# Performance work log

Hardware: AMD Instinct MI355X
Metric: run time of the kernel (lower is better)

Reference implementation:

```python
import jax, jax.numpy as jnp
import numpy as np
from jax import lax

SEQ, BATCH, IN_W = 2048, 64, 256
STREAM_W = 1024
OUT_W = 64


def _range(num, lo, hi):
    return np.arange(num, dtype=np.float64) / float(num - 1) * (hi - lo) + lo


def _sin_buffers(width):
    # Faithful to ResSin: tau = 2*pi, w_min = -2*tau, w_max = 2*tau
    tau = 2.0 * np.pi
    w_max = 2.0 * tau
    l_num = width // 2
    r_num = width - l_num
    inner = np.concatenate([
        _range(l_num, -w_max, -1.0 / l_num),
        _range(r_num, 1.0 / r_num, w_max),
    ])
    outer = np.concatenate([
        _range(l_num, -1.0, -w_max),
        _range(r_num, w_max, 1.0),
    ]) / inner
    return inner.astype(np.float32), outer.astype(np.float32)


def setup_inputs() -> dict:
    key = jax.random.key(0)
    ks = jax.random.split(key, 7)
    W = STREAM_W
    inner, outer = _sin_buffers(W)
    scale = 1.0 / np.sqrt(W)
    return {
        "input": jax.random.normal(ks[0], (SEQ, BATCH, IN_W), dtype=jnp.float32),
        "initial_stream": jax.random.normal(ks[1], (W,), dtype=jnp.float32) * 0.02,
        "w1": jax.random.normal(ks[2], (W, W), dtype=jnp.float32) * scale,
        "b1": jax.random.normal(ks[3], (W,), dtype=jnp.float32) * 0.01,
        "w2": jax.random.normal(ks[4], (W, W), dtype=jnp.float32) * scale,
        "b2": jax.random.normal(ks[5], (W,), dtype=jnp.float32) * 0.01,
        "bendiness": jax.random.normal(ks[6], (W,), dtype=jnp.float32) * 0.1,
        "inner_weight": jnp.asarray(inner),
        "outer_weight": jnp.asarray(outer),
    }


def reference(input, initial_stream, w1, b1, w2, b2, bendiness, inner_weight, outer_weight):
    S, B, I = input.shape
    W = initial_stream.shape[0]
    pad = W - I
    stream0 = jnp.broadcast_to(initial_stream, (B, W))

    def step(stream, elem):
        # Add: pad input element up to stream width and add residually
        s = stream + jnp.pad(elem, ((0, 0), (0, pad)))
        # ResLinear fc1: addmm(bias, x, weight.T)
        h = s @ w1.T + b1
        # ResSin: x + bendiness * outer * sin(x * inner)
        h = h + bendiness * outer_weight * jnp.sin(h * inner_weight)
        # ResLinear fc2
        s = h @ w2.T + b2
        return s, None

    final, _ = lax.scan(step, stream0, input)
    # seq_indices = -1 (default): every batch element takes the last stream
    outputs = final[:, :OUT_W]
    return outputs, final
```

## Files before the change

### kernel.cpp

```cpp
#include <hip/hip_runtime.h>
#include <math.h>


#define WDIM 1024
#define SEQ_N 2048
#define NB 256
#define LDS_BYTES 163840

__device__ __forceinline__ double gload(const double* p) {
  unsigned long long v = __hip_atomic_load((const unsigned long long*)p,
                                           __ATOMIC_RELAXED, __HIP_MEMORY_SCOPE_AGENT);
  return __builtin_bit_cast(double, v);
}
__device__ __forceinline__ void gstore(double* p, double d) {
  __hip_atomic_store((unsigned long long*)p, __builtin_bit_cast(unsigned long long, d),
                     __ATOMIC_RELAXED, __HIP_MEMORY_SCOPE_AGENT);
}

__device__ __forceinline__ void gbar(unsigned* bar, unsigned target, int leaf) {
  __syncthreads();
  if (threadIdx.x == 0) {
    __builtin_amdgcn_fence(__ATOMIC_RELEASE, "agent");
    unsigned old = __hip_atomic_fetch_add(&bar[32 + leaf * 16], 1u, __ATOMIC_RELAXED,
                                          __HIP_MEMORY_SCOPE_AGENT);
    if (old + 1u == target * 16u) {
      unsigned r = __hip_atomic_fetch_add(&bar[16], 1u, __ATOMIC_RELAXED,
                                          __HIP_MEMORY_SCOPE_AGENT);
      if (r + 1u == target * 16u)
        __hip_atomic_store(&bar[0], target, __ATOMIC_RELAXED, __HIP_MEMORY_SCOPE_AGENT);
    }
    while (__hip_atomic_load(&bar[0], __ATOMIC_RELAXED, __HIP_MEMORY_SCOPE_AGENT) < target)
      __builtin_amdgcn_s_sleep(2);
  }
  __syncthreads();
}

__global__ __launch_bounds__(256) void k_gemm_wt(const float* __restrict__ A,
                                                 const float* __restrict__ B,
                                                 double* __restrict__ Wcd) {
  __shared__ float As[32][68];
  __shared__ float Bs[32][68];
  const int tid = threadIdx.x;
  const int tx = tid & 15, ty = tid >> 4;
  const int bx = blockIdx.x, by = blockIdx.y;
  double acc[4][4] = {};
  for (int j0 = 0; j0 < WDIM; j0 += 32) {
    for (int l = tid; l < 64 * 32; l += 256) {
      int r = l >> 5, c = l & 31;
      As[c][r] = A[(by * 64 + r) * WDIM + j0 + c];
    }
    for (int l = tid; l < 32 * 64; l += 256) {
      int r = l >> 6, c = l & 63;
      Bs[r][c] = B[(j0 + r) * WDIM + bx * 64 + c];
    }
    __syncthreads();
#pragma unroll 8
    for (int kk = 0; kk < 32; ++kk) {
      float a[4], bb[4];
      *(float4*)a  = *(const float4*)&As[kk][ty * 4];
      *(float4*)bb = *(const float4*)&Bs[kk][tx * 4];
#pragma unroll
      for (int i = 0; i < 4; ++i)
#pragma unroll
        for (int j = 0; j < 4; ++j) acc[i][j] += (double)a[i] * (double)bb[j];
    }
    __syncthreads();
  }
#pragma unroll
  for (int i = 0; i < 4; ++i)
#pragma unroll
    for (int j = 0; j < 4; ++j)
      Wcd[(size_t)(by * 64 + ty * 4 + i) * WDIM + bx * 64 + tx * 4 + j] = acc[i][j];
}

__global__ __launch_bounds__(256) void k_bias(const float* __restrict__ W1,
                                              const float* __restrict__ b1,
                                              const float* __restrict__ b2,
                                              const float* __restrict__ s0,
                                              double* __restrict__ b1c,
                                              double* __restrict__ c0, unsigned* bar) {
  if (blockIdx.x < 2) {
    int i = blockIdx.x * 256 + threadIdx.x;
    if (i < 288) bar[i] = 0u;
  }
  int wave = threadIdx.x >> 6;
  int lane = threadIdx.x & 63;
  int n = blockIdx.x * 4 + wave;
  const float* row = W1 + (size_t)n * WDIM;
  double a1 = 0.0, a2 = 0.0;
  for (int k = lane; k < WDIM; k += 64) {
    double w = (double)row[k];
    a1 += (double)b2[k] * w;
    a2 += (double)s0[k] * w;
  }
#pragma unroll
  for (int off = 32; off; off >>= 1) {
    a1 += __shfl_down(a1, off, 64);
    a2 += __shfl_down(a2, off, 64);
  }
  if (lane == 0) { b1c[n] = (double)b1[n] + a1; c0[n] = (double)b1[n] + a2; }
}

__global__ __launch_bounds__(512, 2) void k_main(
    const float* __restrict__ x, const double* __restrict__ Wcd,
    const float* __restrict__ W1, const double* __restrict__ b1c,
    const double* __restrict__ c0, const float* __restrict__ W2,
    const float* __restrict__ b2, const float* __restrict__ bend,
    const float* __restrict__ inner, const float* __restrict__ outer,
    double* vA, double* vB, float* __restrict__ out, unsigned* bar) {
  extern __shared__ double2 tile[];
  double* red = (double*)(tile + 8192);
  const int tid = threadIdx.x;
  const int ks = tid & 31;
  const int bg = (tid >> 5) & 3;
  const int ng = (tid >> 7) & 3;
  const int nt = blockIdx.x & 63, g = blockIdx.x >> 6;
  const int leaf = blockIdx.x >> 4;

  if (tid < 256) vA[blockIdx.x * 256 + tid] = 0.0;

  const double* wrow[4];
  const float* w1row[4];
  const float* w2row[4];
#pragma unroll
  for (int jn = 0; jn < 4; ++jn) {
    int n = nt * 16 + ng * 4 + jn;
    wrow[jn]  = Wcd + (size_t)n * WDIM;
    w1row[jn] = W1 + (size_t)n * WDIM;
    w2row[jn] = W2 + (size_t)n * WDIM;
  }

  const int n_red = nt * 16 + (tid & 15);
  const int b_red = g * 16 + ((tid >> 4) & 15);
  const double bo   = (double)bend[n_red] * (double)outer[n_red];
  const double inw  = (double)inner[n_red];
  const double b1cr = b1c[n_red];
  const double c0r  = c0[n_red];
  const int oswz = (ng * 4) & 15;

  unsigned gent = 0;
  double* vin = vA;
  double* vout = vB;
  gbar(bar, ++gent, leaf);

  for (int t = 0; t < SEQ_N; ++t) {
    float2 xv[4][4], wv[4][4];
#pragma unroll
    for (int i = 0; i < 4; ++i) {
      int c2 = i * 32 + ks;
#pragma unroll
      for (int r = 0; r < 4; ++r)
        xv[r][i] = ((const float2*)(x + ((size_t)t * 64 + g * 16 + bg * 4 + r) * 256))[c2];
#pragma unroll
      for (int jn = 0; jn < 4; ++jn)
        wv[jn][i] = ((const float2*)w1row[jn])[c2];
    }
    double va[16], vb[16];
    {
      const double* srcb = vin + (size_t)(g * 16) * WDIM + tid * 2;
#pragma unroll
      for (int j = 0; j < 16; ++j) {
        va[j] = gload(srcb + (size_t)j * WDIM);
        vb[j] = gload(srcb + (size_t)j * WDIM + 1);
      }
    }

    double accx[4][4], accy[4][4];
#pragma unroll
    for (int ib = 0; ib < 4; ++ib)
#pragma unroll
      for (int jn = 0; jn < 4; ++jn) { accx[ib][jn] = 0.0; accy[ib][jn] = 0.0; }
#pragma unroll
    for (int i = 0; i < 4; ++i)
#pragma unroll
      for (int jn = 0; jn < 4; ++jn) {
        double wx = (double)wv[jn][i].x, wy = (double)wv[jn][i].y;
        accx[0][jn] += (double)xv[0][i].x * wx; accy[0][jn] += (double)xv[0][i].y * wy;
        accx[1][jn] += (double)xv[1][i].x * wx; accy[1][jn] += (double)xv[1][i].y * wy;
        accx[2][jn] += (double)xv[2][i].x * wx; accy[2][jn] += (double)xv[2][i].y * wy;
        accx[3][jn] += (double)xv[3][i].x * wx; accy[3][jn] += (double)xv[3][i].y * wy;
      }

#pragma unroll
    for (int j = 0; j < 16; ++j)
      tile[j * 512 + tid] = make_double2(va[j], vb[j]);
    __syncthreads();

#pragma unroll 4
    for (int i = 0; i < 16; ++i) {
      int c2 = i * 32 + ks;
      double2 v0 = tile[(bg * 4 + 0) * 512 + c2];
      double2 v1 = tile[(bg * 4 + 1) * 512 + c2];
      double2 v2 = tile[(bg * 4 + 2) * 512 + c2];
      double2 v3 = tile[(bg * 4 + 3) * 512 + c2];
#pragma unroll
      for (int jn = 0; jn < 4; ++jn) {
        double2 w = ((const double2*)wrow[jn])[c2];
        accx[0][jn] += v0.x * w.x; accy[0][jn] += v0.y * w.y;
        accx[1][jn] += v1.x * w.x; accy[1][jn] += v1.y * w.y;
        accx[2][jn] += v2.x * w.x; accy[2][jn] += v2.y * w.y;
        accx[3][jn] += v3.x * w.x; accy[3][jn] += v3.y * w.y;
      }
    }

#pragma unroll
    for (int ib = 0; ib < 4; ++ib)
#pragma unroll
      for (int jn = 0; jn < 4; ++jn) {
        double p = accx[ib][jn] + accy[ib][jn];
        p += __shfl_xor(p, 16, 64);
        if (ks < 16) {
          int o = (bg * 4 + ib) * 16 + ng * 4 + jn;
          red[o * 16 + (ks ^ ((oswz + jn) & 15))] = p;
        }
      }
    __syncthreads();

    if (tid < 256) {
      double s = 0.0;
      const int oc = tid & 15;
#pragma unroll
      for (int slc = 0; slc < 16; ++slc)
        s += red[tid * 16 + (slc ^ oc)];
      double u = s + (t == 0 ? c0r : b1cr);
      double gv = u + bo * sin(u * inw);
      gstore(&vout[(size_t)b_red * WDIM + n_red], gv);
    }

    gbar(bar, ++gent, leaf);
    double* tmp = vin; vin = vout; vout = tmp;
  }

  {
    double va[16], vb[16];
    {
      const double* srcb = vin + (size_t)(g * 16) * WDIM + tid * 2;
#pragma unroll
      for (int j = 0; j < 16; ++j) {
        va[j] = gload(srcb + (size_t)j * WDIM);
        vb[j] = gload(srcb + (size_t)j * WDIM + 1);
      }
    }
#pragma unroll
    for (int j = 0; j < 16; ++j)
      tile[j * 512 + tid] = make_double2(va[j], vb[j]);
    __syncthreads();

    double accx[4][4], accy[4][4];
#pragma unroll
    for (int ib = 0; ib < 4; ++ib)
#pragma unroll
      for (int jn = 0; jn < 4; ++jn) { accx[ib][jn] = 0.0; accy[ib][jn] = 0.0; }

#pragma unroll 4
    for (int i = 0; i < 16; ++i) {
      int c2 = i * 32 + ks;
      double2 v0 = tile[(bg * 4 + 0) * 512 + c2];
      double2 v1 = tile[(bg * 4 + 1) * 512 + c2];
      double2 v2 = tile[(bg * 4 + 2) * 512 + c2];
      double2 v3 = tile[(bg * 4 + 3) * 512 + c2];
#pragma unroll
      for (int jn = 0; jn < 4; ++jn) {
        float2 wf = ((const float2*)w2row[jn])[c2];
        double wx = (double)wf.x, wy = (double)wf.y;
        accx[0][jn] += v0.x * wx; accy[0][jn] += v0.y * wy;
        accx[1][jn] += v1.x * wx; accy[1][jn] += v1.y * wy;
        accx[2][jn] += v2.x * wx; accy[2][jn] += v2.y * wy;
        accx[3][jn] += v3.x * wx; accy[3][jn] += v3.y * wy;
      }
    }
#pragma unroll
    for (int ib = 0; ib < 4; ++ib)
#pragma unroll
      for (int jn = 0; jn < 4; ++jn) {
        double p = accx[ib][jn] + accy[ib][jn];
        p += __shfl_xor(p, 16, 64);
        if (ks < 16) {
          int o = (bg * 4 + ib) * 16 + ng * 4 + jn;
          red[o * 16 + (ks ^ ((oswz + jn) & 15))] = p;
        }
      }
    __syncthreads();
    if (tid < 256) {
      double s = 0.0;
      const int oc = tid & 15;
#pragma unroll
      for (int slc = 0; slc < 16; ++slc)
        s += red[tid * 16 + (slc ^ oc)];
      double sv = s + (double)b2[n_red];
      out[4096 + (size_t)b_red * WDIM + n_red] = (float)sv;
      if (n_red < 64) out[(size_t)b_red * 64 + n_red] = (float)sv;
    }
  }
}

extern "C" void kernel_launch(void* const* d_in, const int* in_sizes, int n_in,
                              void* d_out, int out_size, void* d_ws, size_t ws_size,
                              hipStream_t stream) {
  const float* x    = (const float*)d_in[0];
  const float* s0   = (const float*)d_in[1];
  const float* W1   = (const float*)d_in[2];
  const float* b1   = (const float*)d_in[3];
  const float* W2   = (const float*)d_in[4];
  const float* b2   = (const float*)d_in[5];
  const float* bend = (const float*)d_in[6];
  const float* inner= (const float*)d_in[7];
  const float* outer= (const float*)d_in[8];
  double* ws = (double*)d_ws;

  double* Wcd = ws;
  double* b1c = ws + 1048576;
  double* c0  = ws + 1049600;
  double* vA  = ws + 1050624;
  double* vB  = ws + 1116160;
  unsigned* bar = (unsigned*)(ws + 1181696);
  float* out = (float*)d_out;

  k_gemm_wt<<<dim3(16, 16), 256, 0, stream>>>(W1, W2, Wcd);
  k_bias<<<256, 256, 0, stream>>>(W1, b1, b2, s0, b1c, c0, bar);

  static bool attr_done = false;
  if (!attr_done) {
    hipFuncSetAttribute((const void*)k_main,
                        hipFuncAttributeMaxDynamicSharedMemorySize, LDS_BYTES);
    attr_done = true;
  }

  void* args[] = { (void*)&x, (void*)&Wcd, (void*)&W1, (void*)&b1c, (void*)&c0,
                   (void*)&W2, (void*)&b2, (void*)&bend, (void*)&inner, (void*)&outer,
                   (void*)&vA, (void*)&vB, (void*)&out, (void*)&bar };
  hipError_t le = hipLaunchCooperativeKernel((void*)k_main, dim3(NB), dim3(512),
                                             args, LDS_BYTES, stream);
  if (le != hipSuccess) {
    k_main<<<dim3(NB), dim3(512), LDS_BYTES, stream>>>(
        x, Wcd, W1, b1c, c0, W2, b2, bend, inner, outer, vA, vB, out, bar);
  }
}
```

Baseline: 36.74 ms.

## Split cooperative kernel into per-batch-group barriers with smaller 256-thread blocks

```diff
diff --git a/kernel.cpp b/kernel.cpp
--- a/kernel.cpp
+++ b/kernel.cpp
@@ -4,8 +4,8 @@
 
 #define WDIM 1024
 #define SEQ_N 2048
-#define NB 256
-#define LDS_BYTES 163840
+#define LDS8 81920
+#define LDSL 163840
 
 __device__ __forceinline__ double gload(const double* p) {
   unsigned long long v = __hip_atomic_load((const unsigned long long*)p,
@@ -17,19 +17,20 @@
                      __ATOMIC_RELAXED, __HIP_MEMORY_SCOPE_AGENT);
 }
 
-__device__ __forceinline__ void gbar(unsigned* bar, unsigned target, int leaf) {
+__device__ __forceinline__ void gbar(unsigned* barR, unsigned target, int leaf,
+                                     unsigned perleaf, unsigned leaves) {
   __syncthreads();
   if (threadIdx.x == 0) {
     __builtin_amdgcn_fence(__ATOMIC_RELEASE, "agent");
-    unsigned old = __hip_atomic_fetch_add(&bar[32 + leaf * 16], 1u, __ATOMIC_RELAXED,
+    unsigned old = __hip_atomic_fetch_add(&barR[32 + leaf * 16], 1u, __ATOMIC_RELAXED,
                                           __HIP_MEMORY_SCOPE_AGENT);
-    if (old + 1u == target * 16u) {
-      unsigned r = __hip_atomic_fetch_add(&bar[16], 1u, __ATOMIC_RELAXED,
+    if (old + 1u == target * perleaf) {
+      unsigned r = __hip_atomic_fetch_add(&barR[16], 1u, __ATOMIC_RELAXED,
                                           __HIP_MEMORY_SCOPE_AGENT);
-      if (r + 1u == target * 16u)
-        __hip_atomic_store(&bar[0], target, __ATOMIC_RELAXED, __HIP_MEMORY_SCOPE_AGENT);
-    }
-    while (__hip_atomic_load(&bar[0], __ATOMIC_RELAXED, __HIP_MEMORY_SCOPE_AGENT) < target)
+      if (r + 1u == target * leaves)
+        __hip_atomic_store(&barR[0], target, __ATOMIC_RELAXED, __HIP_MEMORY_SCOPE_AGENT);
+    }
+    while (__hip_atomic_load(&barR[0], __ATOMIC_RELAXED, __HIP_MEMORY_SCOPE_AGENT) < target)
       __builtin_amdgcn_s_sleep(2);
   }
   __syncthreads();
@@ -79,10 +80,7 @@
                                               const float* __restrict__ s0,
                                               double* __restrict__ b1c,
                                               double* __restrict__ c0, unsigned* bar) {
-  if (blockIdx.x < 2) {
-    int i = blockIdx.x * 256 + threadIdx.x;
-    if (i < 288) bar[i] = 0u;
-  }
+  if (blockIdx.x < 16) bar[blockIdx.x * 256 + threadIdx.x] = 0u;
   int wave = threadIdx.x >> 6;
   int lane = threadIdx.x & 63;
   int n = blockIdx.x * 4 + wave;
@@ -99,6 +97,194 @@
     a2 += __shfl_down(a2, off, 64);
   }
   if (lane == 0) { b1c[n] = (double)b1[n] + a1; c0[n] = (double)b1[n] + a2; }
+}
+
+__global__ __launch_bounds__(256, 2) void k_main8(
+    const float* __restrict__ x, const double* __restrict__ Wcd,
+    const float* __restrict__ W1, const double* __restrict__ b1c,
+    const double* __restrict__ c0, const float* __restrict__ W2,
+    const float* __restrict__ b2, const float* __restrict__ bend,
+    const float* __restrict__ inner, const float* __restrict__ outer,
+    double* vA, double* vB, float* __restrict__ out, unsigned* bar) {
+  extern __shared__ double2 tile[];
+  double* red = (double*)(tile + 4096);
+  const int tid = threadIdx.x;
+  const int ks = tid & 31;
+  const int bg = (tid >> 5) & 1;
+  const int ng = tid >> 6;
+  const int nt = blockIdx.x & 63, g = blockIdx.x >> 6;
+  const int leaf = nt >> 3;
+  unsigned* barG = bar + g * 512;
+
+  if (tid < 128) vA[blockIdx.x * 128 + tid] = 0.0;
+
+  const double* wrow[4];
+  const float* w1row[4];
+  const float* w2row[4];
+#pragma unroll
+  for (int jn = 0; jn < 4; ++jn) {
+    int n = nt * 16 + ng * 4 + jn;
+    wrow[jn]  = Wcd + (size_t)n * WDIM;
+    w1row[jn] = W1 + (size_t)n * WDIM;
+    w2row[jn] = W2 + (size_t)n * WDIM;
+  }
+
+  const int n_red = nt * 16 + (tid & 15);
+  const int b_red = g * 8 + ((tid >> 4) & 7);
+  const double bo   = (double)bend[n_red] * (double)outer[n_red];
+  const double inw  = (double)inner[n_red];
+  const double b1cr = b1c[n_red];
+  const double c0r  = c0[n_red];
+  const int oswz = (ng * 4) & 15;
+
+  unsigned gent = 0;
+  double* vin = vA;
+  double* vout = vB;
+  gbar(barG, ++gent, leaf, 8u, 8u);
+
+  for (int t = 0; t < SEQ_N; ++t) {
+    float2 xv[4][4], wv[4][4];
+#pragma unroll
+    for (int i = 0; i < 4; ++i) {
+      int c2 = i * 32 + ks;
+#pragma unroll
+      for (int r = 0; r < 4; ++r)
+        xv[r][i] = ((const float2*)(x + ((size_t)t * 64 + g * 8 + bg * 4 + r) * 256))[c2];
+#pragma unroll
+      for (int jn = 0; jn < 4; ++jn)
+        wv[jn][i] = ((const float2*)w1row[jn])[c2];
+    }
+    double va[16], vb[16];
+    {
+#pragma unroll
+      for (int j = 0; j < 16; ++j) {
+        int idx = j * 256 + tid;
+        int r = idx >> 9, c2 = idx & 511;
+        const double* s = vin + (size_t)(g * 8 + r) * WDIM + c2 * 2;
+        va[j] = gload(s); vb[j] = gload(s + 1);
+      }
+    }
+    double accx[4][4], accy[4][4];
+#pragma unroll
+    for (int ib = 0; ib < 4; ++ib)
+#pragma unroll
+      for (int jn = 0; jn < 4; ++jn) { accx[ib][jn] = 0.0; accy[ib][jn] = 0.0; }
+#pragma unroll
+    for (int i = 0; i < 4; ++i)
+#pragma unroll
+      for (int jn = 0; jn < 4; ++jn) {
+        double wx = (double)wv[jn][i].x, wy = (double)wv[jn][i].y;
+        accx[0][jn] += (double)xv[0][i].x * wx; accy[0][jn] += (double)xv[0][i].y * wy;
+        accx[1][jn] += (double)xv[1][i].x * wx; accy[1][jn] += (double)xv[1][i].y * wy;
+        accx[2][jn] += (double)xv[2][i].x * wx; accy[2][jn] += (double)xv[2][i].y * wy;
+        accx[3][jn] += (double)xv[3][i].x * wx; accy[3][jn] += (double)xv[3][i].y * wy;
+      }
+#pragma unroll
+    for (int j = 0; j < 16; ++j) {
+      int idx = j * 256 + tid;
+      tile[idx] = make_double2(va[j], vb[j]);
+    }
+    __syncthreads();
+#pragma unroll 4
+    for (int i = 0; i < 16; ++i) {
+      int c2 = i * 32 + ks;
+      double2 v0 = tile[(bg * 4 + 0) * 512 + c2];
+      double2 v1 = tile[(bg * 4 + 1) * 512 + c2];
+      double2 v2 = tile[(bg * 4 + 2) * 512 + c2];
+      double2 v3 = tile[(bg * 4 + 3) * 512 + c2];
+#pragma unroll
+      for (int jn = 0; jn < 4; ++jn) {
+        double2 w = ((const double2*)wrow[jn])[c2];
+        accx[0][jn] += v0.x * w.x; accy[0][jn] += v0.y * w.y;
+        accx[1][jn] += v1.x * w.x; accy[1][jn] += v1.y * w.y;
+        accx[2][jn] += v2.x * w.x; accy[2][jn] += v2.y * w.y;
+        accx[3][jn] += v3.x * w.x; accy[3][jn] += v3.y * w.y;
+      }
+    }
+#pragma unroll
+    for (int ib = 0; ib < 4; ++ib)
+#pragma unroll
+      for (int jn = 0; jn < 4; ++jn) {
+        double p = accx[ib][jn] + accy[ib][jn];
+        p += __shfl_xor(p, 16, 64);
+        if (ks < 16) {
+          int o = (bg * 4 + ib) * 16 + ng * 4 + jn;
+          red[o * 16 + (ks ^ ((oswz + jn) & 15))] = p;
+        }
+      }
+    __syncthreads();
+    if (tid < 128) {
+      double s = 0.0;
+      const int oc = tid & 15;
+#pragma unroll
+      for (int slc = 0; slc < 16; ++slc)
+        s += red[tid * 16 + (slc ^ oc)];
+      double u = s + (t == 0 ? c0r : b1cr);
+      double gv = u + bo * sin(u * inw);
+      gstore(&vout[(size_t)b_red * WDIM + n_red], gv);
+    }
+    gbar(barG, ++gent, leaf, 8u, 8u);
+    double* tmp = vin; vin = vout; vout = tmp;
+  }
+
+  {
+    double va[16], vb[16];
+#pragma unroll
+    for (int j = 0; j < 16; ++j) {
+      int idx = j * 256 + tid;
+      int r = idx >> 9, c2 = idx & 511;
+      const double* s = vin + (size_t)(g * 8 + r) * WDIM + c2 * 2;
+      va[j] = gload(s); vb[j] = gload(s + 1);
+    }
+#pragma unroll
+    for (int j = 0; j < 16; ++j)
+      tile[j * 256 + tid] = make_double2(va[j], vb[j]);
+    __syncthreads();
+    double accx[4][4], accy[4][4];
+#pragma unroll
+    for (int ib = 0; ib < 4; ++ib)
+#pragma unroll
+      for (int jn = 0; jn < 4; ++jn) { accx[ib][jn] = 0.0; accy[ib][jn] = 0.0; }
+#pragma unroll 4
+    for (int i = 0; i < 16; ++i) {
+      int c2 = i * 32 + ks;
+      double2 v0 = tile[(bg * 4 + 0) * 512 + c2];
+      double2 v1 = tile[(bg * 4 + 1) * 512 + c2];
+      double2 v2 = tile[(bg * 4 + 2) * 512 + c2];
+      double2 v3 = tile[(bg * 4 + 3) * 512 + c2];
+#pragma unroll
+      for (int jn = 0; jn < 4; ++jn) {
+        float2 wf = ((const float2*)w2row[jn])[c2];
+        double wx = (double)wf.x, wy = (double)wf.y;
+        accx[0][jn] += v0.x * wx; accy[0][jn] += v0.y * wy;
+        accx[1][jn] += v1.x * wx; accy[1][jn] += v1.y * wy;
+        accx[2][jn] += v2.x * wx; accy[2][jn] += v2.y * wy;
+        accx[3][jn] += v3.x * wx; accy[3][jn] += v3.y * wy;
+      }
+    }
+#pragma unroll
+    for (int ib = 0; ib < 4; ++ib)
+#pragma unroll
+      for (int jn = 0; jn < 4; ++jn) {
+        double p = accx[ib][jn] + accy[ib][jn];
+        p += __shfl_xor(p, 16, 64);
+        if (ks < 16) {
+          int o = (bg * 4 + ib) * 16 + ng * 4 + jn;
+          red[o * 16 + (ks ^ ((oswz + jn) & 15))] = p;
+        }
+      }
+    __syncthreads();
+    if (tid < 128) {
+      double s = 0.0;
+      const int oc = tid & 15;
+#pragma unroll
+      for (int slc = 0; slc < 16; ++slc)
+        s += red[tid * 16 + (slc ^ oc)];
+      double sv = s + (double)b2[n_red];
+      out[4096 + (size_t)b_red * WDIM + n_red] = (float)sv;
+      if (n_red < 64) out[(size_t)b_red * 64 + n_red] = (float)sv;
+    }
+  }
 }
 
 __global__ __launch_bounds__(512, 2) void k_main(
@@ -129,7 +315,6 @@
     w1row[jn] = W1 + (size_t)n * WDIM;
     w2row[jn] = W2 + (size_t)n * WDIM;
   }
-
   const int n_red = nt * 16 + (tid & 15);
   const int b_red = g * 16 + ((tid >> 4) & 15);
   const double bo   = (double)bend[n_red] * (double)outer[n_red];
@@ -141,7 +326,7 @@
   unsigned gent = 0;
   double* vin = vA;
   double* vout = vB;
-  gbar(bar, ++gent, leaf);
+  gbar(bar, ++gent, leaf, 16u, 16u);
 
   for (int t = 0; t < SEQ_N; ++t) {
     float2 xv[4][4], wv[4][4];
@@ -164,7 +349,6 @@
         vb[j] = gload(srcb + (size_t)j * WDIM + 1);
       }
     }
-
     double accx[4][4], accy[4][4];
 #pragma unroll
     for (int ib = 0; ib < 4; ++ib)
@@ -180,12 +364,10 @@
         accx[2][jn] += (double)xv[2][i].x * wx; accy[2][jn] += (double)xv[2][i].y * wy;
         accx[3][jn] += (double)xv[3][i].x * wx; accy[3][jn] += (double)xv[3][i].y * wy;
       }
-
 #pragma unroll
     for (int j = 0; j < 16; ++j)
       tile[j * 512 + tid] = make_double2(va[j], vb[j]);
     __syncthreads();
-
 #pragma unroll 4
     for (int i = 0; i < 16; ++i) {
       int c2 = i * 32 + ks;
@@ -202,7 +384,6 @@
         accx[3][jn] += v3.x * w.x; accy[3][jn] += v3.y * w.y;
       }
     }
-
 #pragma unroll
     for (int ib = 0; ib < 4; ++ib)
 #pragma unroll
@@ -215,7 +396,6 @@
         }
       }
     __syncthreads();
-
     if (tid < 256) {
       double s = 0.0;
       const int oc = tid & 15;
@@ -226,11 +406,9 @@
       double gv = u + bo * sin(u * inw);
       gstore(&vout[(size_t)b_red * WDIM + n_red], gv);
     }
-
-    gbar(bar, ++gent, leaf);
+    gbar(bar, ++gent, leaf, 16u, 16u);
     double* tmp = vin; vin = vout; vout = tmp;
   }
-
   {
     double va[16], vb[16];
     {
@@ -245,13 +423,11 @@
     for (int j = 0; j < 16; ++j)
       tile[j * 512 + tid] = make_double2(va[j], vb[j]);
     __syncthreads();
-
     double accx[4][4], accy[4][4];
 #pragma unroll
     for (int ib = 0; ib < 4; ++ib)
 #pragma unroll
       for (int jn = 0; jn < 4; ++jn) { accx[ib][jn] = 0.0; accy[ib][jn] = 0.0; }
-
 #pragma unroll 4
     for (int i = 0; i < 16; ++i) {
       int c2 = i * 32 + ks;
@@ -321,18 +497,26 @@
 
   static bool attr_done = false;
   if (!attr_done) {
-    hipFuncSetAttribute((const void*)k_main,
-                        hipFuncAttributeMaxDynamicSharedMemorySize, LDS_BYTES);
+    hipFuncSetAttribute((const void*)k_main8, hipFuncAttributeMaxDynamicSharedMemorySize, LDS8);
+    hipFuncSetAttribute((const void*)k_main,  hipFuncAttributeMaxDynamicSharedMemorySize, LDSL);
     attr_done = true;
   }
 
   void* args[] = { (void*)&x, (void*)&Wcd, (void*)&W1, (void*)&b1c, (void*)&c0,
                    (void*)&W2, (void*)&b2, (void*)&bend, (void*)&inner, (void*)&outer,
                    (void*)&vA, (void*)&vB, (void*)&out, (void*)&bar };
-  hipError_t le = hipLaunchCooperativeKernel((void*)k_main, dim3(NB), dim3(512),
-                                             args, LDS_BYTES, stream);
-  if (le != hipSuccess) {
-    k_main<<<dim3(NB), dim3(512), LDS_BYTES, stream>>>(
-        x, Wcd, W1, b1c, c0, W2, b2, bend, inner, outer, vA, vB, out, bar);
-  }
-}
+
+  int maxB8 = 0;
+  hipError_t q8 = hipOccupancyMaxActiveBlocksPerMultiprocessor(&maxB8, k_main8, 256, LDS8);
+  if (q8 == hipSuccess && maxB8 >= 2) {
+    if (hipLaunchCooperativeKernel((void*)k_main8, dim3(512), dim3(256), args,
+                                   LDS8, stream) != hipSuccess)
+      k_main8<<<dim3(512), dim3(256), LDS8, stream>>>(
+          x, Wcd, W1, b1c, c0, W2, b2, bend, inner, outer, vA, vB, out, bar);
+  } else {
+    if (hipLaunchCooperativeKernel((void*)k_main, dim3(256), dim3(512), args,
+                                   LDSL, stream) != hipSuccess)
+      k_main<<<dim3(256), dim3(512), LDSL, stream>>>(
+          x, Wcd, W1, b1c, c0, W2, b2, bend, inner, outer, vA, vB, out, bar);
+  }
+}
```

After: 36.60 ms, median of 2. Within noise of the previous version (-0.4%).

## Replace tree grid barrier with split arrive/wait counter and overlap next-step input GEMV

Applied to the files above, without the earlier changes.

```diff
diff --git a/kernel.cpp b/kernel.cpp
--- a/kernel.cpp
+++ b/kernel.cpp
@@ -16,23 +16,14 @@
   __hip_atomic_store((unsigned long long*)p, __builtin_bit_cast(unsigned long long, d),
                      __ATOMIC_RELAXED, __HIP_MEMORY_SCOPE_AGENT);
 }
-
-__device__ __forceinline__ void gbar(unsigned* bar, unsigned target, int leaf) {
-  __syncthreads();
-  if (threadIdx.x == 0) {
-    __builtin_amdgcn_fence(__ATOMIC_RELEASE, "agent");
-    unsigned old = __hip_atomic_fetch_add(&bar[32 + leaf * 16], 1u, __ATOMIC_RELAXED,
-                                          __HIP_MEMORY_SCOPE_AGENT);
-    if (old + 1u == target * 16u) {
-      unsigned r = __hip_atomic_fetch_add(&bar[16], 1u, __ATOMIC_RELAXED,
-                                          __HIP_MEMORY_SCOPE_AGENT);
-      if (r + 1u == target * 16u)
-        __hip_atomic_store(&bar[0], target, __ATOMIC_RELAXED, __HIP_MEMORY_SCOPE_AGENT);
-    }
-    while (__hip_atomic_load(&bar[0], __ATOMIC_RELAXED, __HIP_MEMORY_SCOPE_AGENT) < target)
-      __builtin_amdgcn_s_sleep(2);
-  }
-  __syncthreads();
+__device__ __forceinline__ double2 ld_l3(const double2* p) {
+  double2 r;
+  asm volatile("global_load_dwordx4 %0, %1, off sc1" : "=v"(r) : "v"(p));
+  return r;
+}
+__device__ __forceinline__ void wait_vm0() {
+  asm volatile("s_waitcnt vmcnt(0)" ::: "memory");
+  __builtin_amdgcn_sched_barrier(0);
 }
 
 __global__ __launch_bounds__(256) void k_gemm_wt(const float* __restrict__ A,
@@ -79,10 +70,7 @@
                                               const float* __restrict__ s0,
                                               double* __restrict__ b1c,
                                               double* __restrict__ c0, unsigned* bar) {
-  if (blockIdx.x < 2) {
-    int i = blockIdx.x * 256 + threadIdx.x;
-    if (i < 288) bar[i] = 0u;
-  }
+  if (blockIdx.x < 4) bar[blockIdx.x * 256 + threadIdx.x] = 0u;
   int wave = threadIdx.x >> 6;
   int lane = threadIdx.x & 63;
   int n = blockIdx.x * 4 + wave;
@@ -115,9 +103,9 @@
   const int bg = (tid >> 5) & 3;
   const int ng = (tid >> 7) & 3;
   const int nt = blockIdx.x & 63, g = blockIdx.x >> 6;
-  const int leaf = blockIdx.x >> 4;
-
-  if (tid < 256) vA[blockIdx.x * 256 + tid] = 0.0;
+  unsigned* cnt = &bar[0];
+
+  if (tid < 256) gstore(&vA[blockIdx.x * 256 + tid], 0.0);
 
   const double* wrow[4];
   const float* w1row[4];
@@ -138,12 +126,7 @@
   const double c0r  = c0[n_red];
   const int oswz = (ng * 4) & 15;
 
-  unsigned gent = 0;
-  double* vin = vA;
-  double* vout = vB;
-  gbar(bar, ++gent, leaf);
-
-  for (int t = 0; t < SEQ_N; ++t) {
+  auto XSEED = [&](int t, double (&aox)[4][4], double (&aoy)[4][4]) {
     float2 xv[4][4], wv[4][4];
 #pragma unroll
     for (int i = 0; i < 4; ++i) {
@@ -155,35 +138,48 @@
       for (int jn = 0; jn < 4; ++jn)
         wv[jn][i] = ((const float2*)w1row[jn])[c2];
     }
-    double va[16], vb[16];
-    {
-      const double* srcb = vin + (size_t)(g * 16) * WDIM + tid * 2;
-#pragma unroll
-      for (int j = 0; j < 16; ++j) {
-        va[j] = gload(srcb + (size_t)j * WDIM);
-        vb[j] = gload(srcb + (size_t)j * WDIM + 1);
-      }
-    }
-
-    double accx[4][4], accy[4][4];
 #pragma unroll
     for (int ib = 0; ib < 4; ++ib)
 #pragma unroll
-      for (int jn = 0; jn < 4; ++jn) { accx[ib][jn] = 0.0; accy[ib][jn] = 0.0; }
+      for (int jn = 0; jn < 4; ++jn) { aox[ib][jn] = 0.0; aoy[ib][jn] = 0.0; }
 #pragma unroll
     for (int i = 0; i < 4; ++i)
 #pragma unroll
       for (int jn = 0; jn < 4; ++jn) {
         double wx = (double)wv[jn][i].x, wy = (double)wv[jn][i].y;
-        accx[0][jn] += (double)xv[0][i].x * wx; accy[0][jn] += (double)xv[0][i].y * wy;
-        accx[1][jn] += (double)xv[1][i].x * wx; accy[1][jn] += (double)xv[1][i].y * wy;
-        accx[2][jn] += (double)xv[2][i].x * wx; accy[2][jn] += (double)xv[2][i].y * wy;
-        accx[3][jn] += (double)xv[3][i].x * wx; accy[3][jn] += (double)xv[3][i].y * wy;
-      }
-
+        aox[0][jn] += (double)xv[0][i].x * wx; aoy[0][jn] += (double)xv[0][i].y * wy;
+        aox[1][jn] += (double)xv[1][i].x * wx; aoy[1][jn] += (double)xv[1][i].y * wy;
+        aox[2][jn] += (double)xv[2][i].x * wx; aoy[2][jn] += (double)xv[2][i].y * wy;
+        aox[3][jn] += (double)xv[3][i].x * wx; aoy[3][jn] += (double)xv[3][i].y * wy;
+      }
+  };
+
+  double aAx[4][4], aAy[4][4], aBx[4][4], aBy[4][4];
+
+  __syncthreads();
+  if (tid == 0) {
+    __builtin_amdgcn_fence(__ATOMIC_RELEASE, "agent");
+    __hip_atomic_fetch_add(cnt, 1u, __ATOMIC_RELAXED, __HIP_MEMORY_SCOPE_AGENT);
+  }
+  XSEED(0, aAx, aAy);
+  if (tid == 0) {
+    while (__hip_atomic_load(cnt, __ATOMIC_RELAXED, __HIP_MEMORY_SCOPE_AGENT) < 256u)
+      __builtin_amdgcn_s_sleep(1);
+  }
+  __syncthreads();
+
+  auto STEP = [&](int t, double (&aix)[4][4], double (&aiy)[4][4],
+                  double (&aox)[4][4], double (&aoy)[4][4],
+                  double* vin, double* vout) {
+    double2 vld[16];
+    const double2* srcb = (const double2*)(vin + (size_t)(g * 16) * WDIM) + tid;
 #pragma unroll
     for (int j = 0; j < 16; ++j)
-      tile[j * 512 + tid] = make_double2(va[j], vb[j]);
+      vld[j] = ld_l3(srcb + j * (WDIM / 2));
+    wait_vm0();
+#pragma unroll
+    for (int j = 0; j < 16; ++j)
+      tile[j * 512 + tid] = vld[j];
     __syncthreads();
 
 #pragma unroll 4
@@ -196,18 +192,17 @@
 #pragma unroll
       for (int jn = 0; jn < 4; ++jn) {
         double2 w = ((const double2*)wrow[jn])[c2];
-        accx[0][jn] += v0.x * w.x; accy[0][jn] += v0.y * w.y;
-        accx[1][jn] += v1.x * w.x; accy[1][jn] += v1.y * w.y;
-        accx[2][jn] += v2.x * w.x; accy[2][jn] += v2.y * w.y;
-        accx[3][jn] += v3.x * w.x; accy[3][jn] += v3.y * w.y;
-      }
-    }
-
+        aix[0][jn] += v0.x * w.x; aiy[0][jn] += v0.y * w.y;
+        aix[1][jn] += v1.x * w.x; aiy[1][jn] += v1.y * w.y;
+        aix[2][jn] += v2.x * w.x; aiy[2][jn] += v2.y * w.y;
+        aix[3][jn] += v3.x * w.x; aiy[3][jn] += v3.y * w.y;
+      }
+    }
 #pragma unroll
     for (int ib = 0; ib < 4; ++ib)
 #pragma unroll
       for (int jn = 0; jn < 4; ++jn) {
-        double p = accx[ib][jn] + accy[ib][jn];
+        double p = aix[ib][jn] + aiy[ib][jn];
         p += __shfl_xor(p, 16, 64);
         if (ks < 16) {
           int o = (bg * 4 + ib) * 16 + ng * 4 + jn;
@@ -215,7 +210,6 @@
         }
       }
     __syncthreads();
-
     if (tid < 256) {
       double s = 0.0;
       const int oc = tid & 15;
@@ -226,15 +220,29 @@
       double gv = u + bo * sin(u * inw);
       gstore(&vout[(size_t)b_red * WDIM + n_red], gv);
     }
-
-    gbar(bar, ++gent, leaf);
-    double* tmp = vin; vin = vout; vout = tmp;
+    __syncthreads();
+    if (tid == 0) {
+      __builtin_amdgcn_fence(__ATOMIC_RELEASE, "agent");
+      __hip_atomic_fetch_add(cnt, 1u, __ATOMIC_RELAXED, __HIP_MEMORY_SCOPE_AGENT);
+    }
+    if (t + 1 < SEQ_N) XSEED(t + 1, aox, aoy);
+    if (tid == 0) {
+      unsigned tgt = (unsigned)(t + 2) * 256u;
+      while (__hip_atomic_load(cnt, __ATOMIC_RELAXED, __HIP_MEMORY_SCOPE_AGENT) < tgt)
+        __builtin_amdgcn_s_sleep(1);
+    }
+    __syncthreads();
+  };
+
+  for (int t = 0; t < SEQ_N; t += 2) {
+    STEP(t,     aAx, aAy, aBx, aBy, vA, vB);
+    STEP(t + 1, aBx, aBy, aAx, aAy, vB, vA);
   }
 
   {
     double va[16], vb[16];
     {
-      const double* srcb = vin + (size_t)(g * 16) * WDIM + tid * 2;
+      const double* srcb = vA + (size_t)(g * 16) * WDIM + tid * 2;
 #pragma unroll
       for (int j = 0; j < 16; ++j) {
         va[j] = gload(srcb + (size_t)j * WDIM);
@@ -245,13 +253,11 @@
     for (int j = 0; j < 16; ++j)
       tile[j * 512 + tid] = make_double2(va[j], vb[j]);
     __syncthreads();
-
     double accx[4][4], accy[4][4];
 #pragma unroll
     for (int ib = 0; ib < 4; ++ib)
 #pragma unroll
       for (int jn = 0; jn < 4; ++jn) { accx[ib][jn] = 0.0; accy[ib][jn] = 0.0; }
-
 #pragma unroll 4
     for (int i = 0; i < 16; ++i) {
       int c2 = i * 32 + ks;
@@ -321,17 +327,15 @@
 
   static bool attr_done = false;
   if (!attr_done) {
-    hipFuncSetAttribute((const void*)k_main,
-                        hipFuncAttributeMaxDynamicSharedMemorySize, LDS_BYTES);
+    hipFuncSetAttribute((const void*)k_main, hipFuncAttributeMaxDynamicSharedMemorySize, LDS_BYTES);
     attr_done = true;
   }
 
   void* args[] = { (void*)&x, (void*)&Wcd, (void*)&W1, (void*)&b1c, (void*)&c0,
                    (void*)&W2, (void*)&b2, (void*)&bend, (void*)&inner, (void*)&outer,
                    (void*)&vA, (void*)&vB, (void*)&out, (void*)&bar };
-  hipError_t le = hipLaunchCooperativeKernel((void*)k_main, dim3(NB), dim3(512),
-                                             args, LDS_BYTES, stream);
-  if (le != hipSuccess) {
+  if (hipLaunchCooperativeKernel((void*)k_main, dim3(NB), dim3(512), args,
+                                 LDS_BYTES, stream) != hipSuccess) {
     k_main<<<dim3(NB), dim3(512), LDS_BYTES, stream>>>(
         x, Wcd, W1, b1c, c0, W2, b2, bend, inner, outer, vA, vB, out, bar);
   }
```

New measurement: 95.06 ms. +158.7%, slower.
